# Performance work log

Measured on AMD Instinct MI355X. Metric: run time of the kernel, lower is better.

## Reference

```python
import jax, jax.numpy as jnp
import numpy as np

D_MODEL = 512
NUM_HEADS = 8
DEPTH = D_MODEL // NUM_HEADS


def setup_inputs() -> dict:
    key = jax.random.key(0)
    kx, kq, kk, kv, ko = jax.random.split(key, 5)
    scale = 1.0 / np.sqrt(D_MODEL)
    return {
        "x": jax.random.normal(kx, (4, 2048, D_MODEL), dtype=jnp.float32),
        "W_q": jax.random.normal(kq, (D_MODEL, D_MODEL), dtype=jnp.float32) * scale,
        "W_k": jax.random.normal(kk, (D_MODEL, D_MODEL), dtype=jnp.float32) * scale,
        "W_v": jax.random.normal(kv, (D_MODEL, D_MODEL), dtype=jnp.float32) * scale,
        "W_o": jax.random.normal(ko, (D_MODEL, D_MODEL), dtype=jnp.float32) * scale,
    }


def reference(x, W_q, W_k, W_v, W_o):
    B, S, _ = x.shape
    # nn.Linear with weight W: y = x @ W.T
    def split_heads(t):
        return t.reshape(B, S, NUM_HEADS, DEPTH).transpose(0, 2, 1, 3)  # [B,H,S,D]
    Q = split_heads(x @ W_q.T)
    K = split_heads(x @ W_k.T)
    V = split_heads(x @ W_v.T)
    b = -jnp.log(jnp.asarray(S, dtype=jnp.float32))  # -log(seq_len) bias
    inv_sqrt_dk = 1.0 / jnp.sqrt(jnp.asarray(DEPTH, dtype=jnp.float32))
    qk = jnp.einsum('bhqd,bhkd->bhqk', Q, K) * inv_sqrt_dk
    attn = jax.nn.sigmoid(qk + b)  # non-softmax sigmoid attention
    out = jnp.einsum('bhqk,bhkd->bhqd', attn, V)
    out = out.transpose(0, 2, 1, 3).reshape(B, S, D_MODEL)
    return out @ W_o.T
```

## Files before the change

### kernel.cpp

```cpp
#include <hip/hip_runtime.h>
#include <stdint.h>

typedef _Float16 f16x8 __attribute__((ext_vector_type(8)));
typedef _Float16 f16x4 __attribute__((ext_vector_type(4)));
typedef __fp16 h16x2 __attribute__((ext_vector_type(2)));
typedef float f32x4 __attribute__((ext_vector_type(4)));

#define SEQ 2048
#define NHEADS 8

#define GLOAD_LDS16(gp, lp)                                                        \
  __builtin_amdgcn_global_load_lds(                                                \
      (const __attribute__((address_space(1))) void*)(uintptr_t)(const void*)(gp), \
      (__attribute__((address_space(3))) void*)(uintptr_t)(void*)(lp), 16, 0, 0)

__device__ __forceinline__ void barrier_lds() {
  __builtin_amdgcn_s_waitcnt(0xc07f);
  __builtin_amdgcn_s_barrier();
}

__device__ __forceinline__ f16x4 pack4(float a, float b, float c, float d) {
  h16x2 lo = __builtin_amdgcn_cvt_pkrtz(a, b);
  h16x2 hi = __builtin_amdgcn_cvt_pkrtz(c, d);
  f16x4 o;
  o.x = (_Float16)lo.x; o.y = (_Float16)lo.y;
  o.z = (_Float16)hi.x; o.w = (_Float16)hi.y;
  return o;
}

__global__ void cvt_all_kernel(const float* __restrict__ x, const float* __restrict__ wq,
                               const float* __restrict__ wk, const float* __restrict__ wv,
                               const float* __restrict__ wo, _Float16* __restrict__ xh,
                               _Float16* __restrict__ wh) {
  int i = blockIdx.x * 256 + threadIdx.x;
  const float* src;
  _Float16* dst;
  int off;
  if (i < 1048576) {
    src = x; dst = xh; off = i;
  } else {
    int j = i - 1048576;
    int sel = j >> 16;
    off = j & 65535;
    src = (sel == 0) ? wq : (sel == 1) ? wk : (sel == 2) ? wv : wo;
    dst = wh + (size_t)sel * 262144;
  }
  float4 v = ((const float4*)src)[off];
  ((f16x4*)dst)[off] = pack4(v.x, v.y, v.z, v.w);
}

__device__ __forceinline__ void gemm_tile_bt(const _Float16* __restrict__ A,
                                             const _Float16* __restrict__ B,
                                             int m0, int n0,
                                             _Float16* lds,
                                             f32x4 (&acc)[4][4]) {
  const int tid = threadIdx.x;
  const int w = tid >> 6, lane = tid & 63;
  const int wr = w >> 1, wc = w & 1;
  const int lrow = lane & 15, q = lane >> 4;
  const int snb = w * 32 + (lane >> 3);
  const int scb = lane & 7;

#pragma unroll
  for (int i = 0; i < 4; ++i)
#pragma unroll
    for (int j = 0; j < 4; ++j)
#pragma unroll
      for (int r = 0; r < 4; ++r) acc[i][j][r] = 0.f;

#pragma unroll
  for (int t = 0; t < 4; ++t) {
    int n = snb + t * 8;
    int cbg = scb ^ (n & 7);
    GLOAD_LDS16(A + (size_t)(m0 + n) * 512 + cbg * 8, lds + (w * 32 + t * 8) * 64);
    GLOAD_LDS16(B + (size_t)(n0 + n) * 512 + cbg * 8, lds + 8192 + (w * 32 + t * 8) * 64);
  }

  for (int kt = 0; kt < 8; ++kt) {
    __syncthreads();
    if (kt < 7) {
      _Float16* nb = lds + ((kt + 1) & 1) * 16384;
#pragma unroll
      for (int t = 0; t < 4; ++t) {
        int n = snb + t * 8;
        int cbg = scb ^ (n & 7);
        GLOAD_LDS16(A + (size_t)(m0 + n) * 512 + (kt + 1) * 64 + cbg * 8, nb + (w * 32 + t * 8) * 64);
        GLOAD_LDS16(B + (size_t)(n0 + n) * 512 + (kt + 1) * 64 + cbg * 8, nb + 8192 + (w * 32 + t * 8) * 64);
      }
    }
    _Float16* As = lds + (kt & 1) * 16384;
    _Float16* Bs = As + 8192;

    f16x8 af[4][2], bfr[4][2];
#pragma unroll
    for (int i = 0; i < 4; ++i) {
      int m = wr * 64 + i * 16 + lrow;
#pragma unroll
      for (int kk = 0; kk < 2; ++kk) {
        int cb = (kk * 4 + q) ^ (m & 7);
        af[i][kk] = *(const f16x8*)(As + m * 64 + cb * 8);
      }
    }
#pragma unroll
    for (int j = 0; j < 4; ++j) {
      int n = wc * 64 + j * 16 + lrow;
#pragma unroll
      for (int kk = 0; kk < 2; ++kk) {
        int cb = (kk * 4 + q) ^ (n & 7);
        bfr[j][kk] = *(const f16x8*)(Bs + n * 64 + cb * 8);
      }
    }
#pragma unroll
    for (int i = 0; i < 4; ++i)
#pragma unroll
      for (int j = 0; j < 4; ++j) {
        acc[i][j] = __builtin_amdgcn_mfma_f32_16x16x32_f16(af[i][0], bfr[j][0], acc[i][j], 0, 0, 0);
        acc[i][j] = __builtin_amdgcn_mfma_f32_16x16x32_f16(af[i][1], bfr[j][1], acc[i][j], 0, 0, 0);
      }
  }
}

__global__ __launch_bounds__(256, 2) void qkv_kernel(
    const _Float16* __restrict__ xb, const _Float16* __restrict__ Wq,
    const _Float16* __restrict__ Wk, const _Float16* __restrict__ Wv,
    _Float16* __restrict__ Qo, _Float16* __restrict__ Ko, _Float16* __restrict__ Vto) {
  __shared__ _Float16 pool[32768];
  const int z = blockIdx.z;
  f32x4 acc[4][4];
  const int tid = threadIdx.x, w = tid >> 6, lane = tid & 63;
  const int wr = w >> 1, wc = w & 1, lcol = lane & 15, q = lane >> 4;

  if (z < 2) {
    const int m0 = blockIdx.y * 128;
    const int n0 = blockIdx.x * 128;
    gemm_tile_bt((z == 0) ? Wq : Wk, xb, m0, n0, pool, acc);
    _Float16* outp = (z == 0) ? Qo : Ko;
    __syncthreads();
#pragma unroll
    for (int i = 0; i < 4; ++i) {
      int cl = wr * 64 + i * 16 + q * 4;
#pragma unroll
      for (int j = 0; j < 4; ++j) {
        int s = wc * 64 + j * 16 + lcol;
        *(f16x4*)(pool + s * 136 + cl) =
            pack4(acc[i][j][0], acc[i][j][1], acc[i][j][2], acc[i][j][3]);
      }
    }
    __syncthreads();
#pragma unroll
    for (int it = 0; it < 16; ++it) {
      int srow = it * 8 + (tid >> 5);
      int ch = tid & 31;
      f16x4 v = *(const f16x4*)(pool + srow * 136 + ch * 4);
      *(f16x4*)(outp + (size_t)(n0 + srow) * 512 + m0 + ch * 4) = v;
    }
  } else {
    const int m0 = blockIdx.x * 128;
    const int n0 = blockIdx.y * 128;
    gemm_tile_bt(xb, Wv, m0, n0, pool, acc);
    const int bb = m0 >> 11, sl0 = m0 & 2047;
    __syncthreads();
#pragma unroll
    for (int i = 0; i < 4; ++i) {
      int s0 = wr * 64 + i * 16 + q * 4;
#pragma unroll
      for (int j = 0; j < 4; ++j) {
        int c = wc * 64 + j * 16 + lcol;
        *(f16x4*)(pool + c * 136 + s0) =
            pack4(acc[i][j][0], acc[i][j][1], acc[i][j][2], acc[i][j][3]);
      }
    }
    __syncthreads();
#pragma unroll
    for (int it = 0; it < 16; ++it) {
      int crow = it * 8 + (tid >> 5);
      int ch = tid & 31;
      int cg = n0 + crow, h = cg >> 6, d = cg & 63;
      f16x4 v = *(const f16x4*)(pool + crow * 136 + ch * 4);
      *(f16x4*)(Vto + ((size_t)((bb * NHEADS + h) * 64 + d)) * SEQ + sl0 + ch * 4) = v;
    }
  }
}

__global__ __launch_bounds__(256, 2) void attn_kernel(
    const _Float16* __restrict__ Qw, const _Float16* __restrict__ Kw,
    const _Float16* __restrict__ Vtw, _Float16* __restrict__ Ow) {
  __shared__ _Float16 lds[32768];

  const int tid = threadIdx.x, w = tid >> 6, lane = tid & 63;
  const int lrow = lane & 15, q = lane >> 4;

  const int L = blockIdx.x;
  const int xcd = L & 7, slot = L >> 3;
  const int bh = xcd * 4 + (slot >> 4), qt = slot & 15;
  const int b = bh >> 3, h = bh & 7;
  const int q0 = qt * 128;

  const _Float16* Qp = Qw + ((size_t)(b * SEQ + q0)) * 512 + h * 64;
  const _Float16* Kp = Kw + ((size_t)b * SEQ) * 512 + h * 64;
  const _Float16* Vp = Vtw + (size_t)bh * 64 * SEQ;

  const int snb = w * 32 + (lane >> 3), scb = lane & 7;
  const int vnb = w * 16 + (lane >> 4), vcb = lane & 15;

  _Float16* Qs = lds;
#pragma unroll
  for (int t = 0; t < 4; ++t) {
    int n = snb + t * 8;
    int cbg = scb ^ (n & 7);
    GLOAD_LDS16(Qp + (size_t)n * 512 + cbg * 8, Qs + (w * 32 + t * 8) * 64);
  }
  __syncthreads();

  f16x8 qa[2][2];
#pragma unroll
  for (int i = 0; i < 2; ++i) {
    int m = w * 32 + i * 16 + lrow;
#pragma unroll
    for (int kk = 0; kk < 2; ++kk) {
      int cb = (kk * 4 + q) ^ (m & 7);
      qa[i][kk] = *(const f16x8*)(Qs + m * 64 + cb * 8);
    }
  }
  barrier_lds();

#pragma unroll
  for (int t = 0; t < 4; ++t) {
    int n = snb + t * 8;
    int cbg = scb ^ (n & 7);
    GLOAD_LDS16(Kp + (size_t)n * 512 + cbg * 8, lds + (w * 32 + t * 8) * 64);
  }
#pragma unroll
  for (int t = 0; t < 4; ++t) {
    int nv = vnb + t * 4;
    int cbg = vcb ^ (nv & 15);
    GLOAD_LDS16(Vp + (size_t)nv * SEQ + cbg * 8, lds + 8192 + (w * 16 + t * 4) * 128);
  }

  f32x4 oacc[2][4];
#pragma unroll
  for (int i = 0; i < 2; ++i)
#pragma unroll
    for (int j = 0; j < 4; ++j)
#pragma unroll
      for (int r = 0; r < 4; ++r) oacc[i][j][r] = 0.f;

  const float c1 = 0.18033688011112042f;

  for (int kt = 0; kt < 16; ++kt) {
    __syncthreads();
    if (kt < 15) {
      _Float16* nb = lds + ((kt + 1) & 1) * 16384;
#pragma unroll
      for (int t = 0; t < 4; ++t) {
        int n = snb + t * 8;
        int cbg = scb ^ (n & 7);
        GLOAD_LDS16(Kp + (size_t)((kt + 1) * 128 + n) * 512 + cbg * 8, nb + (w * 32 + t * 8) * 64);
      }
#pragma unroll
      for (int t = 0; t < 4; ++t) {
        int nv = vnb + t * 4;
        int cbg = vcb ^ (nv & 15);
        GLOAD_LDS16(Vp + (size_t)nv * SEQ + (kt + 1) * 128 + cbg * 8, nb + 8192 + (w * 16 + t * 4) * 128);
      }
    }
    _Float16* Ksc = lds + (kt & 1) * 16384;
    _Float16* Vtsc = Ksc + 8192;

#pragma unroll
    for (int j = 0; j < 8; ++j) {
      int n = j * 16 + lrow;
      f16x8 k0 = *(const f16x8*)(Ksc + n * 64 + ((q ^ (n & 7)) << 3));
      f16x8 k1 = *(const f16x8*)(Ksc + n * 64 + (((4 + q) ^ (n & 7)) << 3));
      f32x4 s0, s1;
#pragma unroll
      for (int r = 0; r < 4; ++r) { s0[r] = 0.f; s1[r] = 0.f; }
      s0 = __builtin_amdgcn_mfma_f32_16x16x32_f16(k0, qa[0][0], s0, 0, 0, 0);
      s0 = __builtin_amdgcn_mfma_f32_16x16x32_f16(k1, qa[0][1], s0, 0, 0, 0);
      s1 = __builtin_amdgcn_mfma_f32_16x16x32_f16(k0, qa[1][0], s1, 0, 0, 0);
      s1 = __builtin_amdgcn_mfma_f32_16x16x32_f16(k1, qa[1][1], s1, 0, 0, 0);

      float p0[4], p1[4];
#pragma unroll
      for (int r = 0; r < 4; ++r) {
        float wp = __builtin_amdgcn_exp2f(__builtin_fmaf(s0[r], c1, -1.0f));
        float e = wp * 0.0009765625f;
        p0[r] = __builtin_fmaf(wp, __builtin_fmaf(e, e, -e), wp);
        float wp1 = __builtin_amdgcn_exp2f(__builtin_fmaf(s1[r], c1, -1.0f));
        float e1 = wp1 * 0.0009765625f;
        p1[r] = __builtin_fmaf(wp1, __builtin_fmaf(e1, e1, -e1), wp1);
      }
      f16x4 pf0 = pack4(p0[0], p0[1], p0[2], p0[3]);
      f16x4 pf1 = pack4(p1[0], p1[1], p1[2], p1[3]);

#pragma unroll
      for (int j2 = 0; j2 < 4; ++j2) {
        int nv = j2 * 16 + lrow;
        int cb = (j * 2 + (q >> 1)) ^ (nv & 15);
        f16x4 vb = *(const f16x4*)(Vtsc + nv * 128 + (cb << 3) + ((q & 1) << 2));
        oacc[0][j2] = __builtin_amdgcn_mfma_f32_16x16x16f16(pf0, vb, oacc[0][j2], 0, 0, 0);
        oacc[1][j2] = __builtin_amdgcn_mfma_f32_16x16x16f16(pf1, vb, oacc[1][j2], 0, 0, 0);
      }
    }
  }

  barrier_lds();
  _Float16* Ob = lds;
#pragma unroll
  for (int i2 = 0; i2 < 2; ++i2) {
#pragma unroll
    for (int j2 = 0; j2 < 4; ++j2) {
      int d = j2 * 16 + lrow;
#pragma unroll
      for (int r = 0; r < 4; ++r) {
        int row = w * 32 + i2 * 16 + q * 4 + r;
        Ob[row * 72 + d] = (_Float16)(oacc[i2][j2][r] * 0.0009765625f);
      }
    }
  }
  barrier_lds();
#pragma unroll
  for (int it = 0; it < 8; ++it) {
    int row = it * 16 + (tid >> 4);
    int ch = tid & 15;
    f16x4 v = *(const f16x4*)(Ob + row * 72 + ch * 4);
    *(f16x4*)(Ow + (size_t)(b * SEQ + q0 + row) * 512 + h * 64 + ch * 4) = v;
  }
}

__global__ __launch_bounds__(256, 2) void oproj_kernel(
    const _Float16* __restrict__ A, const _Float16* __restrict__ Wo,
    float* __restrict__ out) {
  __shared__ _Float16 pool[32768];
  const int m0 = blockIdx.x * 128, n0 = blockIdx.y * 128;
  f32x4 acc[4][4];
  gemm_tile_bt(A, Wo, m0, n0, pool, acc);

  const int tid = threadIdx.x, w = tid >> 6, lane = tid & 63;
  const int wr = w >> 1, wc = w & 1, lcol = lane & 15, q = lane >> 4;
#pragma unroll
  for (int i = 0; i < 4; ++i) {
    int gm0 = m0 + wr * 64 + i * 16 + q * 4;
#pragma unroll
    for (int j = 0; j < 4; ++j) {
      int gn = n0 + wc * 64 + j * 16 + lcol;
#pragma unroll
      for (int r = 0; r < 4; ++r)
        out[(size_t)(gm0 + r) * 512 + gn] = acc[i][j][r];
    }
  }
}

extern "C" void kernel_launch(void* const* d_in, const int* in_sizes, int n_in,
                              void* d_out, int out_size, void* d_ws, size_t ws_size,
                              hipStream_t stream) {
  const float* x = (const float*)d_in[0];
  const float* Wq = (const float*)d_in[1];
  const float* Wk = (const float*)d_in[2];
  const float* Wv = (const float*)d_in[3];
  const float* Wo = (const float*)d_in[4];
  float* out = (float*)d_out;
  char* ws = (char*)d_ws;

  _Float16* xh = (_Float16*)(ws + 0);
  _Float16* wh = (_Float16*)(ws + 8388608);
  _Float16* Qw = (_Float16*)(ws + 10485760);
  _Float16* Kw = (_Float16*)(ws + 18874368);
  _Float16* Vtw = (_Float16*)(ws + 27262976);
  _Float16* Ow = (_Float16*)(ws + 35651584);

  _Float16* wqh = wh;
  _Float16* wkh = wh + 262144;
  _Float16* wvh = wh + 524288;
  _Float16* woh = wh + 786432;

  cvt_all_kernel<<<5120, 256, 0, stream>>>(x, Wq, Wk, Wv, Wo, xh, wh);
  qkv_kernel<<<dim3(64, 4, 3), 256, 0, stream>>>(xh, wqh, wkh, wvh, Qw, Kw, Vtw);
  attn_kernel<<<512, 256, 0, stream>>>(Qw, Kw, Vtw, Ow);
  oproj_kernel<<<dim3(64, 4), 256, 0, stream>>>(Ow, woh, out);
}
```

Measured before the change: 151.5 us.

## Switch attention kernel to 32x32x16 MFMA tiles with permuted K rows

Recasts the attention QK^T and PV matmuls from 16x16 MFMA instructions to 32x32x16 MFMA, with each wave computing a 32x32 score tile per step. K rows are loaded in a permuted order so the score accumulator layout lines up directly with the A-operand layout PV needs, avoiding a shuffle. This cuts the number of MFMA issues and raises operand reuse per LDS read, at the cost of larger accumulators (more VGPRs) and a reworked output-store mapping.

```diff
diff --git a/kernel.cpp b/kernel.cpp
--- a/kernel.cpp
+++ b/kernel.cpp
@@ -5,6 +5,7 @@
 typedef _Float16 f16x4 __attribute__((ext_vector_type(4)));
 typedef __fp16 h16x2 __attribute__((ext_vector_type(2)));
 typedef float f32x4 __attribute__((ext_vector_type(4)));
+typedef float f32x16 __attribute__((ext_vector_type(16)));
 
 #define SEQ 2048
 #define NHEADS 8
@@ -188,7 +189,7 @@
   __shared__ _Float16 lds[32768];
 
   const int tid = threadIdx.x, w = tid >> 6, lane = tid & 63;
-  const int lrow = lane & 15, q = lane >> 4;
+  const int q31 = lane & 31, hi = lane >> 5;
 
   const int L = blockIdx.x;
   const int xcd = L & 7, slot = L >> 3;
@@ -212,15 +213,12 @@
   }
   __syncthreads();
 
-  f16x8 qa[2][2];
-#pragma unroll
-  for (int i = 0; i < 2; ++i) {
-    int m = w * 32 + i * 16 + lrow;
-#pragma unroll
-    for (int kk = 0; kk < 2; ++kk) {
-      int cb = (kk * 4 + q) ^ (m & 7);
-      qa[i][kk] = *(const f16x8*)(Qs + m * 64 + cb * 8);
-    }
+  f16x8 qb[4];
+  const int qrow = w * 32 + q31;
+#pragma unroll
+  for (int s = 0; s < 4; ++s) {
+    int cb = (s * 2 + hi) ^ (qrow & 7);
+    qb[s] = *(const f16x8*)(Qs + qrow * 64 + cb * 8);
   }
   barrier_lds();
 
@@ -237,13 +235,12 @@
     GLOAD_LDS16(Vp + (size_t)nv * SEQ + cbg * 8, lds + 8192 + (w * 16 + t * 4) * 128);
   }
 
-  f32x4 oacc[2][4];
-#pragma unroll
-  for (int i = 0; i < 2; ++i)
-#pragma unroll
-    for (int j = 0; j < 4; ++j)
-#pragma unroll
-      for (int r = 0; r < 4; ++r) oacc[i][j][r] = 0.f;
+  f32x16 oacc[2];
+  f32x16 z16;
+#pragma unroll
+  for (int r = 0; r < 16; ++r) { z16[r] = 0.f; oacc[0][r] = 0.f; oacc[1][r] = 0.f; }
+
+  const int klp = (q31 & 3) | ((q31 & 4) << 1) | ((q31 & 8) >> 1) | (q31 & 16);
 
   const float c1 = 0.18033688011112042f;
 
@@ -268,54 +265,67 @@
     _Float16* Vtsc = Ksc + 8192;
 
 #pragma unroll
-    for (int j = 0; j < 8; ++j) {
-      int n = j * 16 + lrow;
-      f16x8 k0 = *(const f16x8*)(Ksc + n * 64 + ((q ^ (n & 7)) << 3));
-      f16x8 k1 = *(const f16x8*)(Ksc + n * 64 + (((4 + q) ^ (n & 7)) << 3));
-      f32x4 s0, s1;
-#pragma unroll
-      for (int r = 0; r < 4; ++r) { s0[r] = 0.f; s1[r] = 0.f; }
-      s0 = __builtin_amdgcn_mfma_f32_16x16x32_f16(k0, qa[0][0], s0, 0, 0, 0);
-      s0 = __builtin_amdgcn_mfma_f32_16x16x32_f16(k1, qa[0][1], s0, 0, 0, 0);
-      s1 = __builtin_amdgcn_mfma_f32_16x16x32_f16(k0, qa[1][0], s1, 0, 0, 0);
-      s1 = __builtin_amdgcn_mfma_f32_16x16x32_f16(k1, qa[1][1], s1, 0, 0, 0);
-
-      float p0[4], p1[4];
-#pragma unroll
-      for (int r = 0; r < 4; ++r) {
-        float wp = __builtin_amdgcn_exp2f(__builtin_fmaf(s0[r], c1, -1.0f));
+    for (int m = 0; m < 4; ++m) {
+      const int krow = m * 32 + klp;
+      f16x8 ka[4];
+#pragma unroll
+      for (int s = 0; s < 4; ++s) {
+        int cb = (s * 2 + hi) ^ (krow & 7);
+        ka[s] = *(const f16x8*)(Ksc + krow * 64 + cb * 8);
+      }
+      f16x8 vb[2][2];
+#pragma unroll
+      for (int ww = 0; ww < 2; ++ww)
+#pragma unroll
+        for (int t = 0; t < 2; ++t) {
+          int drow = t * 32 + q31;
+          int g = m * 4 + ww * 2 + hi;
+          int cb = g ^ (drow & 15);
+          vb[ww][t] = *(const f16x8*)(Vtsc + drow * 128 + cb * 8);
+        }
+
+      f32x16 sacc = __builtin_amdgcn_mfma_f32_32x32x16_f16(ka[0], qb[0], z16, 0, 0, 0);
+      sacc = __builtin_amdgcn_mfma_f32_32x32x16_f16(ka[1], qb[1], sacc, 0, 0, 0);
+      sacc = __builtin_amdgcn_mfma_f32_32x32x16_f16(ka[2], qb[2], sacc, 0, 0, 0);
+      sacc = __builtin_amdgcn_mfma_f32_32x32x16_f16(ka[3], qb[3], sacc, 0, 0, 0);
+
+      float p[16];
+#pragma unroll
+      for (int r = 0; r < 16; ++r) {
+        float wp = __builtin_amdgcn_exp2f(__builtin_fmaf(sacc[r], c1, -1.0f));
         float e = wp * 0.0009765625f;
-        p0[r] = __builtin_fmaf(wp, __builtin_fmaf(e, e, -e), wp);
-        float wp1 = __builtin_amdgcn_exp2f(__builtin_fmaf(s1[r], c1, -1.0f));
-        float e1 = wp1 * 0.0009765625f;
-        p1[r] = __builtin_fmaf(wp1, __builtin_fmaf(e1, e1, -e1), wp1);
-      }
-      f16x4 pf0 = pack4(p0[0], p0[1], p0[2], p0[3]);
-      f16x4 pf1 = pack4(p1[0], p1[1], p1[2], p1[3]);
-
-#pragma unroll
-      for (int j2 = 0; j2 < 4; ++j2) {
-        int nv = j2 * 16 + lrow;
-        int cb = (j * 2 + (q >> 1)) ^ (nv & 15);
-        f16x4 vb = *(const f16x4*)(Vtsc + nv * 128 + (cb << 3) + ((q & 1) << 2));
-        oacc[0][j2] = __builtin_amdgcn_mfma_f32_16x16x16f16(pf0, vb, oacc[0][j2], 0, 0, 0);
-        oacc[1][j2] = __builtin_amdgcn_mfma_f32_16x16x16f16(pf1, vb, oacc[1][j2], 0, 0, 0);
-      }
+        p[r] = __builtin_fmaf(wp, __builtin_fmaf(e, e, -e), wp);
+      }
+
+      f16x8 pa[2];
+#pragma unroll
+      for (int ww = 0; ww < 2; ++ww) {
+        h16x2 a0 = __builtin_amdgcn_cvt_pkrtz(p[8 * ww + 0], p[8 * ww + 1]);
+        h16x2 a1 = __builtin_amdgcn_cvt_pkrtz(p[8 * ww + 2], p[8 * ww + 3]);
+        h16x2 a2 = __builtin_amdgcn_cvt_pkrtz(p[8 * ww + 4], p[8 * ww + 5]);
+        h16x2 a3 = __builtin_amdgcn_cvt_pkrtz(p[8 * ww + 6], p[8 * ww + 7]);
+        pa[ww][0] = (_Float16)a0.x; pa[ww][1] = (_Float16)a0.y;
+        pa[ww][2] = (_Float16)a1.x; pa[ww][3] = (_Float16)a1.y;
+        pa[ww][4] = (_Float16)a2.x; pa[ww][5] = (_Float16)a2.y;
+        pa[ww][6] = (_Float16)a3.x; pa[ww][7] = (_Float16)a3.y;
+      }
+
+      oacc[0] = __builtin_amdgcn_mfma_f32_32x32x16_f16(pa[0], vb[0][0], oacc[0], 0, 0, 0);
+      oacc[1] = __builtin_amdgcn_mfma_f32_32x32x16_f16(pa[0], vb[0][1], oacc[1], 0, 0, 0);
+      oacc[0] = __builtin_amdgcn_mfma_f32_32x32x16_f16(pa[1], vb[1][0], oacc[0], 0, 0, 0);
+      oacc[1] = __builtin_amdgcn_mfma_f32_32x32x16_f16(pa[1], vb[1][1], oacc[1], 0, 0, 0);
     }
   }
 
   barrier_lds();
   _Float16* Ob = lds;
 #pragma unroll
-  for (int i2 = 0; i2 < 2; ++i2) {
-#pragma unroll
-    for (int j2 = 0; j2 < 4; ++j2) {
-      int d = j2 * 16 + lrow;
-#pragma unroll
-      for (int r = 0; r < 4; ++r) {
-        int row = w * 32 + i2 * 16 + q * 4 + r;
-        Ob[row * 72 + d] = (_Float16)(oacc[i2][j2][r] * 0.0009765625f);
-      }
+  for (int t = 0; t < 2; ++t) {
+#pragma unroll
+    for (int r = 0; r < 16; ++r) {
+      int row = w * 32 + (r & 3) + ((r >> 2) << 3) + hi * 4;
+      int d = t * 32 + q31;
+      Ob[row * 72 + d] = (_Float16)(oacc[t][r] * 0.0009765625f);
     }
   }
   barrier_lds();
```

After: 149.5 us. No clear change (-1.3%).
